# Performance work log

Hardware: AMD Instinct MI355X
Metric: run time of the kernel (lower is better)

## Reference

```python
import jax, jax.numpy as jnp
import numpy as np
from jax import tree_util as jtu

B, N, DIM = 2, 2048, 512
HEADS, DH = 4, 128
CHUNK = 64
NC = N // CHUNK
DHID = 4 * DH  # expansion_factor 4
MAX_LR = 1.0   # default_step_transform_max_lr


def rms_norm(x, g, eps=1e-6):
    var = jnp.mean(jnp.square(x), axis=-1, keepdims=True)
    return x * jax.lax.rsqrt(var + eps) * g


def mem_model(params, x):
    # ResidualNorm(MemoryMLP depth=2): out = mlp(rmsnorm(x)) + x
    g, w1, w2 = params
    h = rms_norm(x, g)
    h = jax.nn.gelu(jnp.dot(h, w1), approximate=False)
    h = jnp.dot(h, w2)
    return h + x


def _expand(a, leaf):
    # broadcast a per-(b*h) scalar gate over a weight leaf
    return a.reshape(a.shape + (1,) * (leaf.ndim - 1))


def neural_memory(seq, g_store, g_retrieve, Wq, Wk, Wv, Wa, ba, Wm, Wd, bd, Wg, Wc, mem_g, w1, w2):
    xs = rms_norm(seq, g_store)      # store_norm
    xr = rms_norm(seq, g_retrieve)   # retrieve_norm

    def split_heads(t):
        return t.reshape(B, N, HEADS, DH).transpose(0, 2, 1, 3)  # b h n d

    k = split_heads(xs @ Wk)
    v = split_heads(xs @ Wv)
    q = split_heads(xr @ Wq)

    # adaptive per-token lr (sigmoid * max_lr)
    lr = (jax.nn.sigmoid(xs @ Wa + ba) * MAX_LR).transpose(0, 2, 1)  # [B,H,N]
    # per-chunk pooled stats drive momentum + decay gates (AveragePool)
    pooled = xs.reshape(B, NC, CHUNK, DIM).mean(axis=2)              # [B,NC,DIM]
    beta = jax.nn.sigmoid(pooled @ Wm)                               # momentum factor [B,NC,H]
    alpha = 1.0 - jax.nn.sigmoid(pooled @ Wd + bd)                   # weight-retain (1-decay)

    BH = B * HEADS
    k_c = k.reshape(BH, NC, CHUNK, DH)
    v_c = v.reshape(BH, NC, CHUNK, DH)
    q_c = q.reshape(BH, NC, CHUNK, DH)
    lr_c = lr.reshape(BH, NC, CHUNK)
    beta_t = beta.transpose(0, 2, 1).reshape(BH, NC).T   # [NC,BH]
    alpha_t = alpha.transpose(0, 2, 1).reshape(BH, NC).T

    # per-head memory params repeated over batch*heads (per_head_learned_parameters)
    init_params = (
        jnp.broadcast_to(mem_g, (B, HEADS, DH)).reshape(BH, DH),
        jnp.broadcast_to(w1, (B, HEADS, DH, DHID)).reshape(BH, DH, DHID),
        jnp.broadcast_to(w2, (B, HEADS, DHID, DH)).reshape(BH, DHID, DH),
    )

    def chunk_loss(params, kc, vc, lrc):
        pred = mem_model(params, kc)                              # [CHUNK,DH]
        return jnp.sum(jnp.mean(jnp.square(pred - vc), axis=-1) * lrc)

    # per-chunk 'surprise' gradients: vmap over (b*h) and chunks, grads wrt init weights
    grad_fn = jax.grad(chunk_loss)
    grads = jax.vmap(jax.vmap(grad_fn, in_axes=(None, 0, 0, 0)), in_axes=(0, 0, 0, 0))(
        init_params, k_c, v_c, lr_c)
    sur_t = jtu.tree_map(lambda g: jnp.moveaxis(-g, 1, 0), grads)  # [NC,BH,...]

    # momentum recurrence: m_t = beta_t * m_{t-1} + surprise_t
    def mom_step(m, inp):
        b, s = inp
        m = jtu.tree_map(lambda mm, ss: _expand(b, mm) * mm + ss, m, s)
        return m, m
    m0 = jtu.tree_map(lambda t: jnp.zeros_like(t[0]), sur_t)
    _, upd_t = jax.lax.scan(mom_step, m0, (beta_t, sur_t))

    # weight recurrence with decay: w_t = (1-decay_t) * w_{t-1} + m_t
    def w_step(w, inp):
        a, u = inp
        w = jtu.tree_map(lambda ww, uu: _expand(a, ww) * ww + uu, w, u)
        return w, w
    _, w_t = jax.lax.scan(w_step, init_params, (alpha_t, upd_t))

    # causal retrieval: chunk i reads weights updated through chunk i-1
    w_prev = jtu.tree_map(
        lambda wt, w0: jnp.moveaxis(jnp.concatenate([w0[None], wt[:-1]], axis=0), 0, 1),
        w_t, init_params)                                          # [BH,NC,...]

    retrieved = jax.vmap(jax.vmap(mem_model))(w_prev, q_c)         # [BH,NC,CHUNK,DH]
    retrieved = retrieved.reshape(B, HEADS, N, DH)
    gate = jax.nn.sigmoid(xr @ Wg).transpose(0, 2, 1)[..., None]   # retrieve_gate [B,H,N,1]
    retrieved = retrieved * gate
    out = retrieved.transpose(0, 2, 1, 3).reshape(B, N, HEADS * DH) @ Wc  # combine_heads
    return out


def setup_inputs():
    key = jax.random.key(0)
    ks = jax.random.split(key, 12)
    s = 0.02
    f = jnp.float32
    return {
        "seq": jax.random.normal(ks[0], (B, N, DIM), f),
        "g_store": jnp.ones((DIM,), f),
        "g_retrieve": jnp.ones((DIM,), f),
        "Wq": jax.random.normal(ks[1], (DIM, HEADS * DH), f) * s,
        "Wk": jax.random.normal(ks[2], (DIM, HEADS * DH), f) * s,
        "Wv": jax.random.normal(ks[3], (DIM, HEADS * DH), f) * s,
        "Wa": jax.random.normal(ks[4], (DIM, HEADS), f) * s,
        "ba": jnp.zeros((HEADS,), f),
        "Wm": jax.random.normal(ks[5], (DIM, HEADS), f) * s,
        "Wd": jax.random.normal(ks[6], (DIM, HEADS), f) * s,
        "bd": jnp.zeros((HEADS,), f),
        "Wg": jax.random.normal(ks[7], (DIM, HEADS), f) * s,
        "Wc": jax.random.normal(ks[8], (HEADS * DH, DIM), f) * s,
        "mem_g": jnp.ones((DH,), f),
        "w1": jax.random.normal(ks[9], (DH, DHID), f) * (1.0 / np.sqrt(DH)),
        "w2": jax.random.normal(ks[10], (DHID, DH), f) * (1.0 / np.sqrt(DHID)),
    }


def reference(seq, g_store, g_retrieve, Wq, Wk, Wv, Wa, ba, Wm, Wd, bd, Wg, Wc, mem_g, w1, w2):
    return neural_memory(seq, g_store, g_retrieve, Wq, Wk, Wv, Wa, ba, Wm, Wd, bd, Wg, Wc, mem_g, w1, w2)
```

## Files before the change

### kernel.cpp

```cpp
#include <hip/hip_runtime.h>
#include <hip/hip_bf16.h>

#define B_ 2
#define N_ 2048
#define DIM_ 512
#define H_ 4
#define DH_ 128
#define DHID_ 512
#define CH_ 64
#define NC_ 32
#define BH_ 8

typedef __bf16 bf16x8 __attribute__((ext_vector_type(8)));
typedef float f32x4 __attribute__((ext_vector_type(4)));

__device__ __forceinline__ f32x4 MFMA(bf16x8 a, bf16x8 b, f32x4 c) {
    return __builtin_amdgcn_mfma_f32_16x16x32_bf16(a, b, c, 0, 0, 0);
}
__device__ __forceinline__ bf16x8 ld8(const __bf16* p) { return *(const bf16x8*)p; }

__device__ __forceinline__ float sigmoidf_(float x) { return 1.0f / (1.0f + expf(-x)); }

__device__ __forceinline__ float gelu_f(float x) {
    float x2 = x * x;
    float u = x * fmaf(0.0713548163f, x2, 1.5957691216f);
    float E = __expf(u);
    float r = __builtin_amdgcn_rcpf(E + 1.0f);
    return x * (1.0f - r);
}
__device__ __forceinline__ void gelu_fg(float x, float& f, float& g) {
    float x2 = x * x;
    float u = x * fmaf(0.0713548163f, x2, 1.5957691216f);
    float E = __expf(u);
    float r = __builtin_amdgcn_rcpf(E + 1.0f);
    float omr = 1.0f - r;
    f = x * omr;
    float th = 1.0f - 2.0f * r;
    float ap = fmaf(0.1070322244f, x2, 0.7978845608f);
    g = fmaf(0.5f * x * (1.0f - th * th), ap, omr);
}

__global__ __launch_bounds__(256) void rms_kernel(
    const float* __restrict__ seq, const float* __restrict__ gs,
    const float* __restrict__ gr, const float* __restrict__ Wa,
    const float* __restrict__ ba, const float* __restrict__ Wg,
    float* __restrict__ xs,
    __bf16* __restrict__ xsb, __bf16* __restrict__ xrb,
    float* __restrict__ lrb, float* __restrict__ gateb)
{
    const int row = blockIdx.x;
    const int t = threadIdx.x;
    const int wave = t >> 6, lane = t & 63;
    const float* x = seq + (size_t)row * DIM_;
    float v0 = x[t], v1 = x[t + 256];
    float ss = v0 * v0 + v1 * v1;
#pragma unroll
    for (int off = 32; off; off >>= 1) ss += __shfl_xor(ss, off);
    __shared__ float red[4];
    __shared__ float red2[4][8];
    if (lane == 0) red[wave] = ss;
    __syncthreads();
    float tot = red[0] + red[1] + red[2] + red[3];
    float r = rsqrtf(tot * (1.0f / DIM_) + 1e-6f);
    size_t o = (size_t)row * DIM_;
    float a0 = v0 * r * gs[t], a1 = v1 * r * gs[t + 256];
    float b0 = v0 * r * gr[t], b1 = v1 * r * gr[t + 256];
    xs[o + t] = a0; xs[o + t + 256] = a1;
    xsb[o + t] = (__bf16)a0; xsb[o + t + 256] = (__bf16)a1;
    xrb[o + t] = (__bf16)b0; xrb[o + t + 256] = (__bf16)b1;
    float pa[4], pg[4];
#pragma unroll
    for (int h = 0; h < 4; ++h) {
        pa[h] = a0 * Wa[t * 4 + h] + a1 * Wa[(t + 256) * 4 + h];
        pg[h] = b0 * Wg[t * 4 + h] + b1 * Wg[(t + 256) * 4 + h];
    }
#pragma unroll
    for (int h = 0; h < 4; ++h)
#pragma unroll
        for (int off = 32; off; off >>= 1) {
            pa[h] += __shfl_xor(pa[h], off);
            pg[h] += __shfl_xor(pg[h], off);
        }
    if (lane == 0) {
#pragma unroll
        for (int h = 0; h < 4; ++h) {
            red2[wave][h] = pa[h];
            red2[wave][4 + h] = pg[h];
        }
    }
    __syncthreads();
    if (t < 8) {
        float s = red2[0][t] + red2[1][t] + red2[2][t] + red2[3][t];
        int b = row >> 11, n = row & 2047;
        if (t < 4) lrb[(size_t)(b * 4 + t) * N_ + n] = sigmoidf_(s + ba[t]);
        else gateb[(size_t)(b * 4 + (t - 4)) * N_ + n] = sigmoidf_(s);
    }
}

__global__ __launch_bounds__(256) void ba_kernel(
    const float* __restrict__ xs, const float* __restrict__ Wm,
    const float* __restrict__ Wd, const float* __restrict__ bd,
    float* __restrict__ beta, float* __restrict__ alpha)
{
    const int b = blockIdx.x >> 5, ci = blockIdx.x & 31;
    const int t = threadIdx.x;
    const int wave = t >> 6, lane = t & 63;
    const float* base = xs + ((size_t)b * N_ + ci * CH_) * DIM_;
    const int d0 = t * 2;
    float s0 = 0.f, s1 = 0.f;
#pragma unroll 8
    for (int r = 0; r < CH_; ++r) {
        s0 += base[(size_t)r * DIM_ + d0];
        s1 += base[(size_t)r * DIM_ + d0 + 1];
    }
    s0 *= (1.0f / CH_); s1 *= (1.0f / CH_);
    float pm[4], pd[4];
#pragma unroll
    for (int h = 0; h < 4; ++h) {
        pm[h] = s0 * Wm[d0 * 4 + h] + s1 * Wm[(d0 + 1) * 4 + h];
        pd[h] = s0 * Wd[d0 * 4 + h] + s1 * Wd[(d0 + 1) * 4 + h];
    }
#pragma unroll
    for (int h = 0; h < 4; ++h)
#pragma unroll
        for (int off = 32; off; off >>= 1) {
            pm[h] += __shfl_xor(pm[h], off);
            pd[h] += __shfl_xor(pd[h], off);
        }
    __shared__ float red2[4][8];
    if (lane == 0) {
#pragma unroll
        for (int h = 0; h < 4; ++h) {
            red2[wave][h] = pm[h];
            red2[wave][4 + h] = pd[h];
        }
    }
    __syncthreads();
    if (t < 4) {
        float sm = red2[0][t] + red2[1][t] + red2[2][t] + red2[3][t];
        float sd = red2[0][4 + t] + red2[1][4 + t] + red2[2][4 + t] + red2[3][4 + t];
        int bh = b * 4 + t;
        beta[bh * NC_ + ci] = sigmoidf_(sm);
        alpha[bh * NC_ + ci] = 1.0f - sigmoidf_(sd + bd[t]);
    }
}

__global__ __launch_bounds__(256) void prep_kernel(
    const float* __restrict__ w1, const float* __restrict__ w2,
    const float* __restrict__ Wq, const float* __restrict__ Wk,
    const float* __restrict__ Wv, const float* __restrict__ Wc,
    __bf16* __restrict__ w1b, __bf16* __restrict__ w1Tb,
    __bf16* __restrict__ w2b, __bf16* __restrict__ w2Tb,
    __bf16* __restrict__ WqT, __bf16* __restrict__ WkT,
    __bf16* __restrict__ WvT, __bf16* __restrict__ WcT)
{
    int idx = blockIdx.x * 256 + threadIdx.x;
    if (idx < 65536) {
        w1b[idx] = (__bf16)w1[idx];
        int j = idx >> 7, d = idx & 127;
        w1Tb[idx] = (__bf16)w1[(size_t)d * DHID_ + j];
        w2b[idx] = (__bf16)w2[idx];
        int d2 = idx >> 9, j2 = idx & 511;
        w2Tb[idx] = (__bf16)w2[(size_t)j2 * DH_ + d2];
    }
    int n = idx >> 9, k = idx & 511;
    WqT[idx] = (__bf16)Wq[(size_t)k * 512 + n];
    WkT[idx] = (__bf16)Wk[(size_t)k * 512 + n];
    WvT[idx] = (__bf16)Wv[(size_t)k * 512 + n];
    WcT[idx] = (__bf16)Wc[(size_t)k * 512 + n];
}

__global__ __launch_bounds__(256, 4) void proj_kernel(
    const __bf16* __restrict__ xsb, const __bf16* __restrict__ xrb,
    const __bf16* __restrict__ WqT, const __bf16* __restrict__ WkT,
    const __bf16* __restrict__ WvT,
    float* __restrict__ qb, float* __restrict__ kb, float* __restrict__ vb)
{
    const int z = blockIdx.z;
    const __bf16* A = (z == 0) ? xrb : xsb;
    const __bf16* WT = (z == 0) ? WqT : (z == 1 ? WkT : WvT);
    float* out = (z == 0) ? qb : (z == 1 ? kb : vb);
    const int t = threadIdx.x;
    const int wave = t >> 6, lane = t & 63;
    const int lrow = lane & 15, lgrp = lane >> 4;
    const int c0 = blockIdx.x * 64 + wave * 16;
    const int col0 = blockIdx.y * 64;
    f32x4 acc[4];
#pragma unroll
    for (int i = 0; i < 4; ++i) acc[i] = (f32x4)0.f;
    const __bf16* ar = A + (size_t)(c0 + lrow) * 512;
#pragma unroll 4
    for (int k0 = 0; k0 < 512; k0 += 32) {
        bf16x8 av = ld8(ar + k0 + lgrp * 8);
#pragma unroll
        for (int ct = 0; ct < 4; ++ct) {
            bf16x8 bv = ld8(WT + (size_t)(col0 + ct * 16 + lrow) * 512 + k0 + lgrp * 8);
            acc[ct] = MFMA(av, bv, acc[ct]);
        }
    }
#pragma unroll
    for (int ct = 0; ct < 4; ++ct)
#pragma unroll
        for (int r = 0; r < 4; ++r) {
            int row = c0 + lgrp * 4 + r, col = col0 + ct * 16 + lrow;
            int b = row >> 11, n = row & 2047, h = col >> 7, d = col & 127;
            out[((((size_t)(b * H_ + h) * NC_ + (n >> 6)) * CH_) + (n & 63)) * DH_ + d] = acc[ct][r];
        }
}

__global__ __launch_bounds__(256, 4) void gemm_out(
    const __bf16* __restrict__ A, const __bf16* __restrict__ WT, float* __restrict__ out)
{
    const int t = threadIdx.x;
    const int wave = t >> 6, lane = t & 63;
    const int lrow = lane & 15, lgrp = lane >> 4;
    const int c0 = blockIdx.x * 64 + wave * 16;
    const int col0 = blockIdx.y * 64;
    f32x4 acc[4];
#pragma unroll
    for (int i = 0; i < 4; ++i) acc[i] = (f32x4)0.f;
    const __bf16* ar = A + (size_t)(c0 + lrow) * 512;
#pragma unroll 4
    for (int k0 = 0; k0 < 512; k0 += 32) {
        bf16x8 av = ld8(ar + k0 + lgrp * 8);
#pragma unroll
        for (int ct = 0; ct < 4; ++ct) {
            bf16x8 bv = ld8(WT + (size_t)(col0 + ct * 16 + lrow) * 512 + k0 + lgrp * 8);
            acc[ct] = MFMA(av, bv, acc[ct]);
        }
    }
#pragma unroll
    for (int ct = 0; ct < 4; ++ct)
#pragma unroll
        for (int r = 0; r < 4; ++r) {
            int row = c0 + lgrp * 4 + r, col = col0 + ct * 16 + lrow;
            out[(size_t)row * 512 + col] = acc[ct][r];
        }
}

__global__ __launch_bounds__(1024) void grad_kernel(
    const float* __restrict__ kbuf, const float* __restrict__ vbuf,
    const float* __restrict__ lrbuf, const float* __restrict__ memg,
    const __bf16* __restrict__ w1b, const __bf16* __restrict__ w1Tb,
    const __bf16* __restrict__ w2b, const __bf16* __restrict__ w2Tb,
    float* __restrict__ sg, __bf16* __restrict__ sw1, __bf16* __restrict__ sw2)
{
    const int blk = blockIdx.x;
    const int t = threadIdx.x;
    const int w = t >> 6, lane = t & 63;
    const int lrow = lane & 15, lgrp = lane >> 4;
    const int bh = blk >> 5, nc = blk & 31;
    const float* kc = kbuf + (size_t)blk * (CH_ * DH_);
    const float* vc = vbuf + (size_t)blk * (CH_ * DH_);
    const float* lrp = lrbuf + (size_t)bh * N_ + nc * CH_;
    __bf16* sw1_blk = sw1 + (size_t)blk * (DHID_ * DH_);
    __bf16* sw2_blk = sw2 + (size_t)blk * (DHID_ * DH_);

    __shared__ __bf16 h_s[64][136];
    __shared__ __bf16 e_s[64][136];
    __shared__ __bf16 a_s[64][136];
    __shared__ __bf16 dz_s[64][136];
    __shared__ __bf16 hT_s[128][72];
    __shared__ __bf16 eT_s[128][72];
    __shared__ __bf16 aT_s[128][72];
    __shared__ __bf16 dzT_s[128][72];
    __shared__ float r_s[64];
    __shared__ float lr_s[64];
    __shared__ float g_s[128];
    __shared__ float part_s[2][128];

    if (t < 128) g_s[t] = memg[t];
    if (t < 64) lr_s[t] = lrp[t];
    {
        const int c = t >> 4, i8 = t & 15, d0 = i8 * 8;
        float xv[8];
        float ss = 0.f;
#pragma unroll
        for (int i = 0; i < 2; ++i) {
            float4 f = *(const float4*)(kc + (size_t)c * DH_ + d0 + i * 4);
            xv[i * 4 + 0] = f.x; xv[i * 4 + 1] = f.y; xv[i * 4 + 2] = f.z; xv[i * 4 + 3] = f.w;
            ss += f.x * f.x + f.y * f.y + f.z * f.z + f.w * f.w;
        }
        ss += __shfl_xor(ss, 1); ss += __shfl_xor(ss, 2);
        ss += __shfl_xor(ss, 4); ss += __shfl_xor(ss, 8);
        float r = rsqrtf(ss * (1.0f / DH_) + 1e-6f);
        if (i8 == 0) r_s[c] = r;
        __syncthreads();
#pragma unroll
        for (int i = 0; i < 8; ++i)
            h_s[c][d0 + i] = (__bf16)(xv[i] * r * g_s[d0 + i]);
    }
    __syncthreads();
    {
        const int d = t >> 3, c0 = (t & 7) * 8;
#pragma unroll
        for (int i = 0; i < 8; ++i) hT_s[d][c0 + i] = h_s[c0 + i][d];
    }
    __syncthreads();

    const int cs = w & 3, dq = w >> 2;
    const int c0w = cs * 16, q0 = dq * 32;
    f32x4 yacc[2];
    yacc[0] = (f32x4)0.f; yacc[1] = (f32x4)0.f;

    bf16x8 w1r[8], w2r[8];
#pragma unroll
    for (int kt = 0; kt < 4; ++kt)
#pragma unroll
        for (int ct = 0; ct < 2; ++ct)
            w1r[kt * 2 + ct] = ld8(w1Tb + (size_t)(q0 + ct * 16 + lrow) * 128 + kt * 32 + lgrp * 8);

    for (int jt = 0; jt < 4; ++jt) {
        f32x4 zacc[2];
        zacc[0] = (f32x4)0.f; zacc[1] = (f32x4)0.f;
#pragma unroll
        for (int kt = 0; kt < 4; ++kt) {
            bf16x8 av = ld8(&h_s[c0w + lrow][kt * 32 + lgrp * 8]);
            zacc[0] = MFMA(av, w1r[kt * 2 + 0], zacc[0]);
            zacc[1] = MFMA(av, w1r[kt * 2 + 1], zacc[1]);
        }
#pragma unroll
        for (int kt = 0; kt < 4; ++kt)
#pragma unroll
            for (int ct = 0; ct < 2; ++ct)
                w2r[kt * 2 + ct] = ld8(w2Tb + (size_t)(q0 + ct * 16 + lrow) * 512 + jt * 128 + kt * 32 + lgrp * 8);
#pragma unroll
        for (int ct = 0; ct < 2; ++ct)
#pragma unroll
            for (int r = 0; r < 4; ++r)
                a_s[c0w + lgrp * 4 + r][q0 + ct * 16 + lrow] = (__bf16)gelu_f(zacc[ct][r]);
        __syncthreads();
#pragma unroll
        for (int kt = 0; kt < 4; ++kt) {
            bf16x8 av = ld8(&a_s[c0w + lrow][kt * 32 + lgrp * 8]);
            yacc[0] = MFMA(av, w2r[kt * 2 + 0], yacc[0]);
            yacc[1] = MFMA(av, w2r[kt * 2 + 1], yacc[1]);
        }
        if (jt < 3) {
#pragma unroll
            for (int kt = 0; kt < 4; ++kt)
#pragma unroll
                for (int ct = 0; ct < 2; ++ct)
                    w1r[kt * 2 + ct] = ld8(w1Tb + (size_t)((jt + 1) * 128 + q0 + ct * 16 + lrow) * 128 + kt * 32 + lgrp * 8);
        }
        __syncthreads();
    }
#pragma unroll
    for (int ct = 0; ct < 2; ++ct)
#pragma unroll
        for (int r = 0; r < 4; ++r) {
            int c = c0w + lgrp * 4 + r, d = q0 + ct * 16 + lrow;
            float xvv = kc[(size_t)c * DH_ + d];
            float vvv = vc[(size_t)c * DH_ + d];
            float e = lr_s[c] * (2.0f / DH_) * (yacc[ct][r] + xvv - vvv);
            e_s[c][d] = (__bf16)e;
            eT_s[d][c] = (__bf16)e;
        }
    __syncthreads();

    const int js = w & 7, chh = w >> 3;
    f32x4 dhacc[2];
    dhacc[0] = (f32x4)0.f; dhacc[1] = (f32x4)0.f;

    bf16x8 azr[4], adr[4], w1br[4];
#pragma unroll
    for (int kt = 0; kt < 4; ++kt) {
        azr[kt] = ld8(w1Tb + (size_t)(js * 16 + lrow) * 128 + kt * 32 + lgrp * 8);
        adr[kt] = ld8(w2b + (size_t)(js * 16 + lrow) * 128 + kt * 32 + lgrp * 8);
    }

    for (int jt = 0; jt < 4; ++jt) {
        f32x4 ztacc[2], dtacc[2];
        ztacc[0] = (f32x4)0.f; ztacc[1] = (f32x4)0.f;
        dtacc[0] = (f32x4)0.f; dtacc[1] = (f32x4)0.f;
#pragma unroll
        for (int kt = 0; kt < 4; ++kt) {
#pragma unroll
            for (int ct = 0; ct < 2; ++ct) {
                bf16x8 bvh = ld8(&h_s[chh * 32 + ct * 16 + lrow][kt * 32 + lgrp * 8]);
                bf16x8 bve = ld8(&e_s[chh * 32 + ct * 16 + lrow][kt * 32 + lgrp * 8]);
                ztacc[ct] = MFMA(azr[kt], bvh, ztacc[ct]);
                dtacc[ct] = MFMA(adr[kt], bve, dtacc[ct]);
            }
        }
#pragma unroll
        for (int kt = 0; kt < 4; ++kt)
            w1br[kt] = ld8(w1b + (size_t)(js * 16 + lrow) * 512 + jt * 128 + kt * 32 + lgrp * 8);
#pragma unroll
        for (int ct = 0; ct < 2; ++ct)
#pragma unroll
            for (int r = 0; r < 4; ++r) {
                int j = js * 16 + lgrp * 4 + r, c = chh * 32 + ct * 16 + lrow;
                float zt = ztacc[ct][r];
                float gf, gg;
                gelu_fg(zt, gf, gg);
                aT_s[j][c] = (__bf16)gf;
                float dzt = dtacc[ct][r] * gg;
                dzT_s[j][c] = (__bf16)dzt;
                dz_s[c][j] = (__bf16)dzt;
            }
        __syncthreads();
        {
            f32x4 wacc[4];
#pragma unroll
            for (int i = 0; i < 4; ++i) wacc[i] = (f32x4)0.f;
#pragma unroll
            for (int kt = 0; kt < 2; ++kt) {
                bf16x8 av = ld8(&dzT_s[js * 16 + lrow][kt * 32 + lgrp * 8]);
#pragma unroll
                for (int ct = 0; ct < 4; ++ct) {
                    bf16x8 bv = ld8(&hT_s[chh * 64 + ct * 16 + lrow][kt * 32 + lgrp * 8]);
                    wacc[ct] = MFMA(av, bv, wacc[ct]);
                }
            }
#pragma unroll
            for (int ct = 0; ct < 4; ++ct)
#pragma unroll
                for (int r = 0; r < 4; ++r) {
                    int jg = jt * 128 + js * 16 + lgrp * 4 + r, d = chh * 64 + ct * 16 + lrow;
                    sw1_blk[(size_t)jg * 128 + d] = (__bf16)(-wacc[ct][r]);
                }
        }
        {
            f32x4 wacc[4];
#pragma unroll
            for (int i = 0; i < 4; ++i) wacc[i] = (f32x4)0.f;
#pragma unroll
            for (int kt = 0; kt < 2; ++kt) {
                bf16x8 av = ld8(&eT_s[js * 16 + lrow][kt * 32 + lgrp * 8]);
#pragma unroll
                for (int ct = 0; ct < 4; ++ct) {
                    bf16x8 bv = ld8(&aT_s[chh * 64 + ct * 16 + lrow][kt * 32 + lgrp * 8]);
                    wacc[ct] = MFMA(av, bv, wacc[ct]);
                }
            }
#pragma unroll
            for (int ct = 0; ct < 4; ++ct)
#pragma unroll
                for (int r = 0; r < 4; ++r) {
                    int d = js * 16 + lgrp * 4 + r, jg = jt * 128 + chh * 64 + ct * 16 + lrow;
                    sw2_blk[(size_t)d * 512 + jg] = (__bf16)(-wacc[ct][r]);
                }
        }
#pragma unroll
        for (int kt = 0; kt < 4; ++kt) {
#pragma unroll
            for (int ct = 0; ct < 2; ++ct) {
                bf16x8 bv = ld8(&dz_s[chh * 32 + ct * 16 + lrow][kt * 32 + lgrp * 8]);
                dhacc[ct] = MFMA(w1br[kt], bv, dhacc[ct]);
            }
        }
        if (jt < 3) {
#pragma unroll
            for (int kt = 0; kt < 4; ++kt) {
                azr[kt] = ld8(w1Tb + (size_t)((jt + 1) * 128 + js * 16 + lrow) * 128 + kt * 32 + lgrp * 8);
                adr[kt] = ld8(w2b + (size_t)((jt + 1) * 128 + js * 16 + lrow) * 128 + kt * 32 + lgrp * 8);
            }
        }
        __syncthreads();
    }
    {
        float s[4] = {0.f, 0.f, 0.f, 0.f};
#pragma unroll
        for (int ct = 0; ct < 2; ++ct)
#pragma unroll
            for (int r = 0; r < 4; ++r) {
                int d = js * 16 + lgrp * 4 + r, c = chh * 32 + ct * 16 + lrow;
                s[r] += dhacc[ct][r] * (float)hT_s[d][c];
            }
#pragma unroll
        for (int r = 0; r < 4; ++r) {
            s[r] += __shfl_xor(s[r], 1); s[r] += __shfl_xor(s[r], 2);
            s[r] += __shfl_xor(s[r], 4); s[r] += __shfl_xor(s[r], 8);
        }
        if (lrow == 0) {
#pragma unroll
            for (int r = 0; r < 4; ++r) part_s[chh][js * 16 + lgrp * 4 + r] = s[r];
        }
        __syncthreads();
        if (t < 128) sg[(size_t)blk * DH_ + t] = -(part_s[0][t] + part_s[1][t]) / g_s[t];
    }
}

__global__ __launch_bounds__(256) void scan_all(
    __bf16* __restrict__ sw1, const __bf16* __restrict__ w1T,
    __bf16* __restrict__ sw2, const __bf16* __restrict__ w2T,
    float* __restrict__ sgb, const float* __restrict__ memg,
    const float* __restrict__ beta, const float* __restrict__ alpha)
{
    const int bi = blockIdx.x, t = threadIdx.x;
    if (bi < 512) {
        __bf16* buf = (bi < 256) ? sw1 : sw2;
        const __bf16* init = (bi < 256) ? w1T : w2T;
        int idx = (bi & 255) * 256 + t;
        int bh = idx >> 13, e8 = idx & 8191;
        size_t off = (size_t)e8 * 8;
        const float* bp = beta + bh * NC_;
        const float* ap = alpha + bh * NC_;
        __bf16* base = buf + (size_t)bh * NC_ * 65536 + off;
        bf16x8 iv = *(const bf16x8*)(init + off);
        float m[8], wv[8];
#pragma unroll
        for (int k = 0; k < 8; ++k) { m[k] = 0.f; wv[k] = (float)iv[k]; }
        for (int ci = 0; ci < NC_; ++ci) {
            bf16x8 s = *(const bf16x8*)(base + (size_t)ci * 65536);
            float bb = bp[ci], aa = ap[ci];
            bf16x8 o;
#pragma unroll
            for (int k = 0; k < 8; ++k) {
                o[k] = (__bf16)wv[k];
                m[k] = fmaf(bb, m[k], (float)s[k]);
                wv[k] = fmaf(aa, wv[k], m[k]);
            }
            *(bf16x8*)(base + (size_t)ci * 65536) = o;
        }
    } else {
        int idx = (bi - 512) * 256 + t;
        int bh = idx >> 7, el = idx & 127;
        float wv = memg[el], m = 0.f;
        const float* bp = beta + bh * NC_;
        const float* ap = alpha + bh * NC_;
        float* base = sgb + ((size_t)bh * NC_) * 128 + el;
        for (int ci = 0; ci < NC_; ++ci) {
            float s = base[(size_t)ci * 128];
            base[(size_t)ci * 128] = wv;
            m = fmaf(bp[ci], m, s);
            wv = fmaf(ap[ci], wv, m);
        }
    }
}

__global__ __launch_bounds__(512, 4) void retrieve_kernel(
    const float* __restrict__ qbuf, const float* __restrict__ gatebuf,
    const float* __restrict__ sg, const __bf16* __restrict__ sw1,
    const __bf16* __restrict__ sw2, __bf16* __restrict__ retgb)
{
    const int blk = blockIdx.x;
    const int t = threadIdx.x;
    const int w = t >> 6, lane = t & 63;
    const int lrow = lane & 15, lgrp = lane >> 4;
    const int bh = blk >> 5, nc = blk & 31;
    const float* qc = qbuf + (size_t)blk * (CH_ * DH_);
    const __bf16* w1p = sw1 + (size_t)blk * (DHID_ * DH_);
    const __bf16* w2p = sw2 + (size_t)blk * (DHID_ * DH_);
    const float* gp = sg + (size_t)blk * DH_;

    __shared__ __bf16 h_s[64][136];
    __shared__ __bf16 a_s[64][136];
    __shared__ float g_s[128];

    if (t < 128) g_s[t] = gp[t];
    {
        const int c = t >> 3, dblk = t & 7, d0 = dblk * 16;
        float xv[16];
        float ss = 0.f;
#pragma unroll
        for (int i = 0; i < 4; ++i) {
            float4 f = *(const float4*)(qc + (size_t)c * DH_ + d0 + i * 4);
            xv[i * 4 + 0] = f.x; xv[i * 4 + 1] = f.y; xv[i * 4 + 2] = f.z; xv[i * 4 + 3] = f.w;
            ss += f.x * f.x + f.y * f.y + f.z * f.z + f.w * f.w;
        }
        ss += __shfl_xor(ss, 1); ss += __shfl_xor(ss, 2); ss += __shfl_xor(ss, 4);
        float r = rsqrtf(ss * (1.0f / DH_) + 1e-6f);
        __syncthreads();
#pragma unroll
        for (int i = 0; i < 16; ++i)
            h_s[c][d0 + i] = (__bf16)(xv[i] * r * g_s[d0 + i]);
    }
    __syncthreads();

    const int cs = w & 3, dh2 = w >> 2;
    const int c0w = cs * 16, d0w = dh2 * 64;
    f32x4 yacc[4];
#pragma unroll
    for (int i = 0; i < 4; ++i) yacc[i] = (f32x4)0.f;

    for (int jt = 0; jt < 4; ++jt) {
        f32x4 zacc[4];
#pragma unroll
        for (int i = 0; i < 4; ++i) zacc[i] = (f32x4)0.f;
#pragma unroll
        for (int kt = 0; kt < 4; ++kt) {
            bf16x8 av = ld8(&h_s[c0w + lrow][kt * 32 + lgrp * 8]);
#pragma unroll
            for (int ct = 0; ct < 4; ++ct) {
                int j = jt * 128 + d0w + ct * 16 + lrow;
                bf16x8 bv = ld8(w1p + (size_t)j * 128 + kt * 32 + lgrp * 8);
                zacc[ct] = MFMA(av, bv, zacc[ct]);
            }
        }
#pragma unroll
        for (int ct = 0; ct < 4; ++ct)
#pragma unroll
            for (int r = 0; r < 4; ++r)
                a_s[c0w + lgrp * 4 + r][d0w + ct * 16 + lrow] = (__bf16)gelu_f(zacc[ct][r]);
        __syncthreads();
#pragma unroll
        for (int kt = 0; kt < 4; ++kt) {
            bf16x8 av = ld8(&a_s[c0w + lrow][kt * 32 + lgrp * 8]);
#pragma unroll
            for (int ct = 0; ct < 4; ++ct) {
                int d = d0w + ct * 16 + lrow;
                bf16x8 bv = ld8(w2p + (size_t)d * 512 + jt * 128 + kt * 32 + lgrp * 8);
                yacc[ct] = MFMA(av, bv, yacc[ct]);
            }
        }
        __syncthreads();
    }
    const int b = bh >> 2, hh = bh & 3;
#pragma unroll
    for (int ct = 0; ct < 4; ++ct)
#pragma unroll
        for (int r = 0; r < 4; ++r) {
            int c = c0w + lgrp * 4 + r, d = d0w + ct * 16 + lrow;
            int n = nc * CH_ + c;
            float q = qc[(size_t)c * DH_ + d];
            float gv = gatebuf[(size_t)bh * N_ + n];
            retgb[((size_t)(b * N_ + n)) * 512 + hh * 128 + d] = (__bf16)((yacc[ct][r] + q) * gv);
        }
}

extern "C" void kernel_launch(void* const* d_in, const int* in_sizes, int n_in,
                              void* d_out, int out_size, void* d_ws, size_t ws_size,
                              hipStream_t stream) {
    const float* seq     = (const float*)d_in[0];
    const float* g_store = (const float*)d_in[1];
    const float* g_retr  = (const float*)d_in[2];
    const float* Wq = (const float*)d_in[3];
    const float* Wk = (const float*)d_in[4];
    const float* Wv = (const float*)d_in[5];
    const float* Wa = (const float*)d_in[6];
    const float* ba = (const float*)d_in[7];
    const float* Wm = (const float*)d_in[8];
    const float* Wd = (const float*)d_in[9];
    const float* bd = (const float*)d_in[10];
    const float* Wg = (const float*)d_in[11];
    const float* Wc = (const float*)d_in[12];
    const float* memg = (const float*)d_in[13];
    const float* w1 = (const float*)d_in[14];
    const float* w2 = (const float*)d_in[15];
    float* out = (float*)d_out;

    float* p = (float*)d_ws;
    float* xs = p;     p += (size_t)B_ * N_ * DIM_;
    float* kb = p;     p += (size_t)B_ * N_ * DIM_;
    float* vb = p;     p += (size_t)B_ * N_ * DIM_;
    float* qb = p;     p += (size_t)B_ * N_ * DIM_;
    float* lrb = p;    p += (size_t)BH_ * N_;
    float* gateb = p;  p += (size_t)BH_ * N_;
    float* beta = p;   p += BH_ * NC_;
    float* alpha = p;  p += BH_ * NC_;
    float* sgb = p;    p += (size_t)BH_ * NC_ * DH_;

    __bf16* bp_ = (__bf16*)p;
    __bf16* xsb = bp_;  bp_ += (size_t)B_ * N_ * DIM_;
    __bf16* xrb = bp_;  bp_ += (size_t)B_ * N_ * DIM_;
    __bf16* retgb = bp_; bp_ += (size_t)B_ * N_ * DIM_;
    __bf16* w1b = bp_;  bp_ += DH_ * DHID_;
    __bf16* w1Tb = bp_; bp_ += DH_ * DHID_;
    __bf16* w2b = bp_;  bp_ += DH_ * DHID_;
    __bf16* w2Tb = bp_; bp_ += DH_ * DHID_;
    __bf16* WqT = bp_;  bp_ += DIM_ * DIM_;
    __bf16* WkT = bp_;  bp_ += DIM_ * DIM_;
    __bf16* WvT = bp_;  bp_ += DIM_ * DIM_;
    __bf16* WcT = bp_;  bp_ += DIM_ * DIM_;
    __bf16* sw1b = bp_; bp_ += (size_t)BH_ * NC_ * DH_ * DHID_;
    __bf16* sw2b = bp_; bp_ += (size_t)BH_ * NC_ * DH_ * DHID_;

    rms_kernel<<<B_ * N_, 256, 0, stream>>>(seq, g_store, g_retr, Wa, ba, Wg,
                                            xs, xsb, xrb, lrb, gateb);
    ba_kernel<<<B_ * NC_, 256, 0, stream>>>(xs, Wm, Wd, bd, beta, alpha);
    prep_kernel<<<1024, 256, 0, stream>>>(w1, w2, Wq, Wk, Wv, Wc,
                                          w1b, w1Tb, w2b, w2Tb, WqT, WkT, WvT, WcT);
    proj_kernel<<<dim3(64, 8, 3), 256, 0, stream>>>(xsb, xrb, WqT, WkT, WvT, qb, kb, vb);
    grad_kernel<<<BH_ * NC_, 1024, 0, stream>>>(kb, vb, lrb, memg, w1b, w1Tb, w2b, w2Tb,
                                                sgb, sw1b, sw2b);
    scan_all<<<516, 256, 0, stream>>>(sw1b, w1Tb, sw2b, w2Tb, sgb, memg, beta, alpha);
    retrieve_kernel<<<BH_ * NC_, 512, 0, stream>>>(qb, gateb, sgb, sw1b, sw2b, retgb);
    gemm_out<<<dim3(64, 8), 256, 0, stream>>>(retgb, WcT, out);
}
```

Measured before the change: 315.3 us.

## Split grad kernel into hprep, forward and backward kernels with doubled block counts

Replaces the monolithic 256-block grad kernel with three kernels: a normalization prep that writes h and its transpose to global bf16 buffers, a forward kernel that computes the error over half-chunks (512 blocks), and a backward kernel that computes weight gradients over half of the hidden dimension (512 blocks). The aim is more parallelism and lower per-block shared memory on a 256-CU-class GPU, where the old kernel ran only one 1024-thread block per chunk. The norm-gain gradient is now computed algebraically from w1 times the w1 gradient, not from dh, with two partial buffers summed inside the scan. The cost is extra global round-trips for h, e and their transposes, plus two more launches.

After: 474.6 us. +50.5%, slower.

```diff
diff --git a/kernel.cpp b/kernel.cpp
--- a/kernel.cpp
+++ b/kernel.cpp
@@ -238,166 +238,168 @@
         }
 }
 
-__global__ __launch_bounds__(1024) void grad_kernel(
-    const float* __restrict__ kbuf, const float* __restrict__ vbuf,
-    const float* __restrict__ lrbuf, const float* __restrict__ memg,
-    const __bf16* __restrict__ w1b, const __bf16* __restrict__ w1Tb,
-    const __bf16* __restrict__ w2b, const __bf16* __restrict__ w2Tb,
-    float* __restrict__ sg, __bf16* __restrict__ sw1, __bf16* __restrict__ sw2)
+__global__ __launch_bounds__(256) void hprep_kernel(
+    const float* __restrict__ kbuf, const float* __restrict__ memg,
+    __bf16* __restrict__ hb, __bf16* __restrict__ hTb)
 {
     const int blk = blockIdx.x;
+    const int t = threadIdx.x;
+    __shared__ __bf16 h_s[64][130];
+    __shared__ float g_s[128];
+    if (t < 128) g_s[t] = memg[t];
+    const int c = t >> 2, q = t & 3, d0 = q * 32;
+    const float* kc = kbuf + (size_t)blk * 8192 + (size_t)c * 128 + d0;
+    float xv[32];
+    float ss = 0.f;
+#pragma unroll
+    for (int i = 0; i < 8; ++i) {
+        float4 f = *(const float4*)(kc + i * 4);
+        xv[i * 4 + 0] = f.x; xv[i * 4 + 1] = f.y; xv[i * 4 + 2] = f.z; xv[i * 4 + 3] = f.w;
+        ss += f.x * f.x + f.y * f.y + f.z * f.z + f.w * f.w;
+    }
+    ss += __shfl_xor(ss, 1); ss += __shfl_xor(ss, 2);
+    float r = rsqrtf(ss * (1.0f / DH_) + 1e-6f);
+    __syncthreads();
+    bf16x8 pk[4];
+#pragma unroll
+    for (int i = 0; i < 32; ++i) {
+        __bf16 hv = (__bf16)(xv[i] * r * g_s[d0 + i]);
+        h_s[c][d0 + i] = hv;
+        pk[i >> 3][i & 7] = hv;
+    }
+    __bf16* hrow = hb + (size_t)blk * 8192 + (size_t)c * 128 + d0;
+#pragma unroll
+    for (int i = 0; i < 4; ++i) *(bf16x8*)(hrow + i * 8) = pk[i];
+    __syncthreads();
+    const int d = t >> 1, c0 = (t & 1) * 32;
+#pragma unroll
+    for (int i = 0; i < 4; ++i) {
+        bf16x8 o;
+#pragma unroll
+        for (int k = 0; k < 8; ++k) o[k] = h_s[c0 + i * 8 + k][d];
+        *(bf16x8*)(hTb + (size_t)blk * 8192 + (size_t)d * 64 + c0 + i * 8) = o;
+    }
+}
+
+__global__ __launch_bounds__(1024, 8) void gradfwd_kernel(
+    const __bf16* __restrict__ hb, const float* __restrict__ kbuf,
+    const float* __restrict__ vbuf, const float* __restrict__ lrbuf,
+    const __bf16* __restrict__ w1Tb, const __bf16* __restrict__ w2Tb,
+    __bf16* __restrict__ eb, __bf16* __restrict__ eTb)
+{
+    const int bi = blockIdx.x;
+    const int blk = bi >> 1, chalf = bi & 1;
     const int t = threadIdx.x;
     const int w = t >> 6, lane = t & 63;
     const int lrow = lane & 15, lgrp = lane >> 4;
     const int bh = blk >> 5, nc = blk & 31;
-    const float* kc = kbuf + (size_t)blk * (CH_ * DH_);
-    const float* vc = vbuf + (size_t)blk * (CH_ * DH_);
-    const float* lrp = lrbuf + (size_t)bh * N_ + nc * CH_;
+
+    __shared__ __bf16 a_s[32][516];
+    __shared__ float lr_s[32];
+    if (t < 32) lr_s[t] = lrbuf[(size_t)bh * N_ + nc * CH_ + chalf * 32 + t];
+
+    const __bf16* hblk = hb + (size_t)blk * 8192 + (size_t)chalf * 32 * 128;
+
+    {
+        const int cs = w & 1, jq = w >> 1;
+        const int j0 = jq * 64;
+        f32x4 zacc[4];
+#pragma unroll
+        for (int i = 0; i < 4; ++i) zacc[i] = (f32x4)0.f;
+#pragma unroll
+        for (int kt = 0; kt < 4; ++kt) {
+            bf16x8 av = ld8(hblk + (size_t)(cs * 16 + lrow) * 128 + kt * 32 + lgrp * 8);
+#pragma unroll
+            for (int ct = 0; ct < 4; ++ct) {
+                bf16x8 bv = ld8(w1Tb + (size_t)(j0 + ct * 16 + lrow) * 128 + kt * 32 + lgrp * 8);
+                zacc[ct] = MFMA(av, bv, zacc[ct]);
+            }
+        }
+#pragma unroll
+        for (int ct = 0; ct < 4; ++ct)
+#pragma unroll
+            for (int r = 0; r < 4; ++r)
+                a_s[cs * 16 + lgrp * 4 + r][j0 + ct * 16 + lrow] = (__bf16)gelu_f(zacc[ct][r]);
+    }
+    __syncthreads();
+
+    {
+        const int cs = w & 1, dq = w >> 1;
+        const int d0 = dq * 16;
+        f32x4 yacc = (f32x4)0.f;
+#pragma unroll
+        for (int kt = 0; kt < 16; ++kt) {
+            bf16x8 av = ld8(&a_s[cs * 16 + lrow][kt * 32 + lgrp * 8]);
+            bf16x8 bv = ld8(w2Tb + (size_t)(d0 + lrow) * 512 + kt * 32 + lgrp * 8);
+            yacc = MFMA(av, bv, yacc);
+        }
+        const int d = d0 + lrow;
+#pragma unroll
+        for (int r = 0; r < 4; ++r) {
+            int cl = cs * 16 + lgrp * 4 + r;
+            int cc = chalf * 32 + cl;
+            float kv = kbuf[(size_t)blk * 8192 + (size_t)cc * 128 + d];
+            float vv = vbuf[(size_t)blk * 8192 + (size_t)cc * 128 + d];
+            float e = lr_s[cl] * (2.0f / DH_) * (yacc[r] + kv - vv);
+            eb[(size_t)blk * 8192 + (size_t)cc * 128 + d] = (__bf16)e;
+            eTb[(size_t)blk * 8192 + (size_t)d * 64 + cc] = (__bf16)e;
+        }
+    }
+}
+
+__global__ __launch_bounds__(1024, 8) void gradbwd_kernel(
+    const __bf16* __restrict__ hb, const __bf16* __restrict__ hTb,
+    const __bf16* __restrict__ eb, const __bf16* __restrict__ eTb,
+    const __bf16* __restrict__ w1b, const __bf16* __restrict__ w1Tb,
+    const __bf16* __restrict__ w2b,
+    __bf16* __restrict__ sw1, __bf16* __restrict__ sw2,
+    float* __restrict__ sgpA, float* __restrict__ sgpB)
+{
+    const int bi = blockIdx.x;
+    const int blk = bi >> 1, jhalf = bi & 1;
+    const int t = threadIdx.x;
+    const int w = t >> 6, lane = t & 63;
+    const int lrow = lane & 15, lgrp = lane >> 4;
+    const int js = w & 7, chh = w >> 3;
+    const __bf16* hblk = hb + (size_t)blk * 8192;
+    const __bf16* eblk = eb + (size_t)blk * 8192;
+    const __bf16* hTblk = hTb + (size_t)blk * 8192;
+    const __bf16* eTblk = eTb + (size_t)blk * 8192;
     __bf16* sw1_blk = sw1 + (size_t)blk * (DHID_ * DH_);
     __bf16* sw2_blk = sw2 + (size_t)blk * (DHID_ * DH_);
 
-    __shared__ __bf16 h_s[64][136];
-    __shared__ __bf16 e_s[64][136];
-    __shared__ __bf16 a_s[64][136];
-    __shared__ __bf16 dz_s[64][136];
-    __shared__ __bf16 hT_s[128][72];
-    __shared__ __bf16 eT_s[128][72];
-    __shared__ __bf16 aT_s[128][72];
-    __shared__ __bf16 dzT_s[128][72];
-    __shared__ float r_s[64];
-    __shared__ float lr_s[64];
-    __shared__ float g_s[128];
-    __shared__ float part_s[2][128];
-
-    if (t < 128) g_s[t] = memg[t];
-    if (t < 64) lr_s[t] = lrp[t];
-    {
-        const int c = t >> 4, i8 = t & 15, d0 = i8 * 8;
-        float xv[8];
-        float ss = 0.f;
-#pragma unroll
-        for (int i = 0; i < 2; ++i) {
-            float4 f = *(const float4*)(kc + (size_t)c * DH_ + d0 + i * 4);
-            xv[i * 4 + 0] = f.x; xv[i * 4 + 1] = f.y; xv[i * 4 + 2] = f.z; xv[i * 4 + 3] = f.w;
-            ss += f.x * f.x + f.y * f.y + f.z * f.z + f.w * f.w;
-        }
-        ss += __shfl_xor(ss, 1); ss += __shfl_xor(ss, 2);
-        ss += __shfl_xor(ss, 4); ss += __shfl_xor(ss, 8);
-        float r = rsqrtf(ss * (1.0f / DH_) + 1e-6f);
-        if (i8 == 0) r_s[c] = r;
-        __syncthreads();
-#pragma unroll
-        for (int i = 0; i < 8; ++i)
-            h_s[c][d0 + i] = (__bf16)(xv[i] * r * g_s[d0 + i]);
-    }
-    __syncthreads();
-    {
-        const int d = t >> 3, c0 = (t & 7) * 8;
-#pragma unroll
-        for (int i = 0; i < 8; ++i) hT_s[d][c0 + i] = h_s[c0 + i][d];
-    }
-    __syncthreads();
-
-    const int cs = w & 3, dq = w >> 2;
-    const int c0w = cs * 16, q0 = dq * 32;
-    f32x4 yacc[2];
-    yacc[0] = (f32x4)0.f; yacc[1] = (f32x4)0.f;
-
-    bf16x8 w1r[8], w2r[8];
-#pragma unroll
-    for (int kt = 0; kt < 4; ++kt)
-#pragma unroll
-        for (int ct = 0; ct < 2; ++ct)
-            w1r[kt * 2 + ct] = ld8(w1Tb + (size_t)(q0 + ct * 16 + lrow) * 128 + kt * 32 + lgrp * 8);
-
-    for (int jt = 0; jt < 4; ++jt) {
-        f32x4 zacc[2];
-        zacc[0] = (f32x4)0.f; zacc[1] = (f32x4)0.f;
-#pragma unroll
-        for (int kt = 0; kt < 4; ++kt) {
-            bf16x8 av = ld8(&h_s[c0w + lrow][kt * 32 + lgrp * 8]);
-            zacc[0] = MFMA(av, w1r[kt * 2 + 0], zacc[0]);
-            zacc[1] = MFMA(av, w1r[kt * 2 + 1], zacc[1]);
-        }
-#pragma unroll
-        for (int kt = 0; kt < 4; ++kt)
-#pragma unroll
-            for (int ct = 0; ct < 2; ++ct)
-                w2r[kt * 2 + ct] = ld8(w2Tb + (size_t)(q0 + ct * 16 + lrow) * 512 + jt * 128 + kt * 32 + lgrp * 8);
-#pragma unroll
-        for (int ct = 0; ct < 2; ++ct)
-#pragma unroll
-            for (int r = 0; r < 4; ++r)
-                a_s[c0w + lgrp * 4 + r][q0 + ct * 16 + lrow] = (__bf16)gelu_f(zacc[ct][r]);
-        __syncthreads();
-#pragma unroll
-        for (int kt = 0; kt < 4; ++kt) {
-            bf16x8 av = ld8(&a_s[c0w + lrow][kt * 32 + lgrp * 8]);
-            yacc[0] = MFMA(av, w2r[kt * 2 + 0], yacc[0]);
-            yacc[1] = MFMA(av, w2r[kt * 2 + 1], yacc[1]);
-        }
-        if (jt < 3) {
-#pragma unroll
-            for (int kt = 0; kt < 4; ++kt)
-#pragma unroll
-                for (int ct = 0; ct < 2; ++ct)
-                    w1r[kt * 2 + ct] = ld8(w1Tb + (size_t)((jt + 1) * 128 + q0 + ct * 16 + lrow) * 128 + kt * 32 + lgrp * 8);
-        }
-        __syncthreads();
-    }
-#pragma unroll
-    for (int ct = 0; ct < 2; ++ct)
-#pragma unroll
-        for (int r = 0; r < 4; ++r) {
-            int c = c0w + lgrp * 4 + r, d = q0 + ct * 16 + lrow;
-            float xvv = kc[(size_t)c * DH_ + d];
-            float vvv = vc[(size_t)c * DH_ + d];
-            float e = lr_s[c] * (2.0f / DH_) * (yacc[ct][r] + xvv - vvv);
-            e_s[c][d] = (__bf16)e;
-            eT_s[d][c] = (__bf16)e;
-        }
-    __syncthreads();
-
-    const int js = w & 7, chh = w >> 3;
-    f32x4 dhacc[2];
-    dhacc[0] = (f32x4)0.f; dhacc[1] = (f32x4)0.f;
-
-    bf16x8 azr[4], adr[4], w1br[4];
-#pragma unroll
-    for (int kt = 0; kt < 4; ++kt) {
-        azr[kt] = ld8(w1Tb + (size_t)(js * 16 + lrow) * 128 + kt * 32 + lgrp * 8);
-        adr[kt] = ld8(w2b + (size_t)(js * 16 + lrow) * 128 + kt * 32 + lgrp * 8);
-    }
-
-    for (int jt = 0; jt < 4; ++jt) {
+    __shared__ __bf16 aT_s[128][66];
+    __shared__ __bf16 dzT_s[128][66];
+    __shared__ float part_dg[16][64];
+
+    float dgacc[4] = {0.f, 0.f, 0.f, 0.f};
+
+    for (int jt = jhalf * 2; jt < jhalf * 2 + 2; ++jt) {
+        const int jg0 = jt * 128;
         f32x4 ztacc[2], dtacc[2];
         ztacc[0] = (f32x4)0.f; ztacc[1] = (f32x4)0.f;
         dtacc[0] = (f32x4)0.f; dtacc[1] = (f32x4)0.f;
 #pragma unroll
         for (int kt = 0; kt < 4; ++kt) {
+            bf16x8 avz = ld8(w1Tb + (size_t)(jg0 + js * 16 + lrow) * 128 + kt * 32 + lgrp * 8);
+            bf16x8 avd = ld8(w2b + (size_t)(jg0 + js * 16 + lrow) * 128 + kt * 32 + lgrp * 8);
 #pragma unroll
             for (int ct = 0; ct < 2; ++ct) {
-                bf16x8 bvh = ld8(&h_s[chh * 32 + ct * 16 + lrow][kt * 32 + lgrp * 8]);
-                bf16x8 bve = ld8(&e_s[chh * 32 + ct * 16 + lrow][kt * 32 + lgrp * 8]);
-                ztacc[ct] = MFMA(azr[kt], bvh, ztacc[ct]);
-                dtacc[ct] = MFMA(adr[kt], bve, dtacc[ct]);
-            }
-        }
-#pragma unroll
-        for (int kt = 0; kt < 4; ++kt)
-            w1br[kt] = ld8(w1b + (size_t)(js * 16 + lrow) * 512 + jt * 128 + kt * 32 + lgrp * 8);
+                bf16x8 bvh = ld8(hblk + (size_t)(chh * 32 + ct * 16 + lrow) * 128 + kt * 32 + lgrp * 8);
+                bf16x8 bve = ld8(eblk + (size_t)(chh * 32 + ct * 16 + lrow) * 128 + kt * 32 + lgrp * 8);
+                ztacc[ct] = MFMA(avz, bvh, ztacc[ct]);
+                dtacc[ct] = MFMA(avd, bve, dtacc[ct]);
+            }
+        }
 #pragma unroll
         for (int ct = 0; ct < 2; ++ct)
 #pragma unroll
             for (int r = 0; r < 4; ++r) {
-                int j = js * 16 + lgrp * 4 + r, c = chh * 32 + ct * 16 + lrow;
-                float zt = ztacc[ct][r];
+                int jl = js * 16 + lgrp * 4 + r, c = chh * 32 + ct * 16 + lrow;
                 float gf, gg;
-                gelu_fg(zt, gf, gg);
-                aT_s[j][c] = (__bf16)gf;
-                float dzt = dtacc[ct][r] * gg;
-                dzT_s[j][c] = (__bf16)dzt;
-                dz_s[c][j] = (__bf16)dzt;
+                gelu_fg(ztacc[ct][r], gf, gg);
+                aT_s[jl][c] = (__bf16)gf;
+                dzT_s[jl][c] = (__bf16)(dtacc[ct][r] * gg);
             }
         __syncthreads();
         {
@@ -409,17 +411,20 @@
                 bf16x8 av = ld8(&dzT_s[js * 16 + lrow][kt * 32 + lgrp * 8]);
 #pragma unroll
                 for (int ct = 0; ct < 4; ++ct) {
-                    bf16x8 bv = ld8(&hT_s[chh * 64 + ct * 16 + lrow][kt * 32 + lgrp * 8]);
+                    bf16x8 bv = ld8(hTblk + (size_t)(chh * 64 + ct * 16 + lrow) * 64 + kt * 32 + lgrp * 8);
                     wacc[ct] = MFMA(av, bv, wacc[ct]);
                 }
             }
 #pragma unroll
-            for (int ct = 0; ct < 4; ++ct)
+            for (int ct = 0; ct < 4; ++ct) {
+                int d = chh * 64 + ct * 16 + lrow;
 #pragma unroll
                 for (int r = 0; r < 4; ++r) {
-                    int jg = jt * 128 + js * 16 + lgrp * 4 + r, d = chh * 64 + ct * 16 + lrow;
+                    int jg = jg0 + js * 16 + lgrp * 4 + r;
                     sw1_blk[(size_t)jg * 128 + d] = (__bf16)(-wacc[ct][r]);
+                    dgacc[ct] -= (float)w1Tb[(size_t)jg * 128 + d] * wacc[ct][r];
                 }
+            }
         }
         {
             f32x4 wacc[4];
@@ -427,7 +432,7 @@
             for (int i = 0; i < 4; ++i) wacc[i] = (f32x4)0.f;
 #pragma unroll
             for (int kt = 0; kt < 2; ++kt) {
-                bf16x8 av = ld8(&eT_s[js * 16 + lrow][kt * 32 + lgrp * 8]);
+                bf16x8 av = ld8(eTblk + (size_t)(js * 16 + lrow) * 64 + kt * 32 + lgrp * 8);
 #pragma unroll
                 for (int ct = 0; ct < 4; ++ct) {
                     bf16x8 bv = ld8(&aT_s[chh * 64 + ct * 16 + lrow][kt * 32 + lgrp * 8]);
@@ -438,54 +443,37 @@
             for (int ct = 0; ct < 4; ++ct)
 #pragma unroll
                 for (int r = 0; r < 4; ++r) {
-                    int d = js * 16 + lgrp * 4 + r, jg = jt * 128 + chh * 64 + ct * 16 + lrow;
+                    int d = js * 16 + lgrp * 4 + r, jg = jg0 + chh * 64 + ct * 16 + lrow;
                     sw2_blk[(size_t)d * 512 + jg] = (__bf16)(-wacc[ct][r]);
                 }
         }
-#pragma unroll
-        for (int kt = 0; kt < 4; ++kt) {
-#pragma unroll
-            for (int ct = 0; ct < 2; ++ct) {
-                bf16x8 bv = ld8(&dz_s[chh * 32 + ct * 16 + lrow][kt * 32 + lgrp * 8]);
-                dhacc[ct] = MFMA(w1br[kt], bv, dhacc[ct]);
-            }
-        }
-        if (jt < 3) {
-#pragma unroll
-            for (int kt = 0; kt < 4; ++kt) {
-                azr[kt] = ld8(w1Tb + (size_t)((jt + 1) * 128 + js * 16 + lrow) * 128 + kt * 32 + lgrp * 8);
-                adr[kt] = ld8(w2b + (size_t)((jt + 1) * 128 + js * 16 + lrow) * 128 + kt * 32 + lgrp * 8);
-            }
-        }
         __syncthreads();
     }
-    {
-        float s[4] = {0.f, 0.f, 0.f, 0.f};
-#pragma unroll
-        for (int ct = 0; ct < 2; ++ct)
-#pragma unroll
-            for (int r = 0; r < 4; ++r) {
-                int d = js * 16 + lgrp * 4 + r, c = chh * 32 + ct * 16 + lrow;
-                s[r] += dhacc[ct][r] * (float)hT_s[d][c];
-            }
-#pragma unroll
-        for (int r = 0; r < 4; ++r) {
-            s[r] += __shfl_xor(s[r], 1); s[r] += __shfl_xor(s[r], 2);
-            s[r] += __shfl_xor(s[r], 4); s[r] += __shfl_xor(s[r], 8);
-        }
-        if (lrow == 0) {
-#pragma unroll
-            for (int r = 0; r < 4; ++r) part_s[chh][js * 16 + lgrp * 4 + r] = s[r];
-        }
-        __syncthreads();
-        if (t < 128) sg[(size_t)blk * DH_ + t] = -(part_s[0][t] + part_s[1][t]) / g_s[t];
+#pragma unroll
+    for (int ct = 0; ct < 4; ++ct) {
+        dgacc[ct] += __shfl_xor(dgacc[ct], 16);
+        dgacc[ct] += __shfl_xor(dgacc[ct], 32);
+    }
+    if (lane < 16) {
+#pragma unroll
+        for (int ct = 0; ct < 4; ++ct) part_dg[w][ct * 16 + lane] = dgacc[ct];
+    }
+    __syncthreads();
+    if (t < 128) {
+        int grp = t >> 6;
+        float s = 0.f;
+#pragma unroll
+        for (int j = 0; j < 8; ++j) s += part_dg[grp * 8 + j][t & 63];
+        float* dst = jhalf ? sgpB : sgpA;
+        dst[(size_t)blk * DH_ + t] = s;
     }
 }
 
 __global__ __launch_bounds__(256) void scan_all(
     __bf16* __restrict__ sw1, const __bf16* __restrict__ w1T,
     __bf16* __restrict__ sw2, const __bf16* __restrict__ w2T,
-    float* __restrict__ sgb, const float* __restrict__ memg,
+    float* __restrict__ sgb, const float* __restrict__ sgpB,
+    const float* __restrict__ memg,
     const float* __restrict__ beta, const float* __restrict__ alpha)
 {
     const int bi = blockIdx.x, t = threadIdx.x;
@@ -517,12 +505,15 @@
     } else {
         int idx = (bi - 512) * 256 + t;
         int bh = idx >> 7, el = idx & 127;
-        float wv = memg[el], m = 0.f;
+        float g = memg[el];
+        float rg = 1.0f / g;
+        float wv = g, m = 0.f;
         const float* bp = beta + bh * NC_;
         const float* ap = alpha + bh * NC_;
         float* base = sgb + ((size_t)bh * NC_) * 128 + el;
+        const float* baseB = sgpB + ((size_t)bh * NC_) * 128 + el;
         for (int ci = 0; ci < NC_; ++ci) {
-            float s = base[(size_t)ci * 128];
+            float s = (base[(size_t)ci * 128] + baseB[(size_t)ci * 128]) * rg;
             base[(size_t)ci * 128] = wv;
             m = fmaf(bp[ci], m, s);
             wv = fmaf(ap[ci], wv, m);
@@ -651,11 +642,16 @@
     float* beta = p;   p += BH_ * NC_;
     float* alpha = p;  p += BH_ * NC_;
     float* sgb = p;    p += (size_t)BH_ * NC_ * DH_;
+    float* sgpB = p;   p += (size_t)BH_ * NC_ * DH_;
 
     __bf16* bp_ = (__bf16*)p;
     __bf16* xsb = bp_;  bp_ += (size_t)B_ * N_ * DIM_;
     __bf16* xrb = bp_;  bp_ += (size_t)B_ * N_ * DIM_;
     __bf16* retgb = bp_; bp_ += (size_t)B_ * N_ * DIM_;
+    __bf16* hbuf = bp_; bp_ += (size_t)BH_ * N_ * DH_;
+    __bf16* hTbuf = bp_; bp_ += (size_t)BH_ * N_ * DH_;
+    __bf16* ebuf = bp_; bp_ += (size_t)BH_ * N_ * DH_;
+    __bf16* eTbuf = bp_; bp_ += (size_t)BH_ * N_ * DH_;
     __bf16* w1b = bp_;  bp_ += DH_ * DHID_;
     __bf16* w1Tb = bp_; bp_ += DH_ * DHID_;
     __bf16* w2b = bp_;  bp_ += DH_ * DHID_;
@@ -673,9 +669,13 @@
     prep_kernel<<<1024, 256, 0, stream>>>(w1, w2, Wq, Wk, Wv, Wc,
                                           w1b, w1Tb, w2b, w2Tb, WqT, WkT, WvT, WcT);
     proj_kernel<<<dim3(64, 8, 3), 256, 0, stream>>>(xsb, xrb, WqT, WkT, WvT, qb, kb, vb);
-    grad_kernel<<<BH_ * NC_, 1024, 0, stream>>>(kb, vb, lrb, memg, w1b, w1Tb, w2b, w2Tb,
-                                                sgb, sw1b, sw2b);
-    scan_all<<<516, 256, 0, stream>>>(sw1b, w1Tb, sw2b, w2Tb, sgb, memg, beta, alpha);
+    hprep_kernel<<<BH_ * NC_, 256, 0, stream>>>(kb, memg, hbuf, hTbuf);
+    gradfwd_kernel<<<BH_ * NC_ * 2, 1024, 0, stream>>>(hbuf, kb, vb, lrb, w1Tb, w2Tb,
+                                                       ebuf, eTbuf);
+    gradbwd_kernel<<<BH_ * NC_ * 2, 1024, 0, stream>>>(hbuf, hTbuf, ebuf, eTbuf,
+                                                       w1b, w1Tb, w2b,
+                                                       sw1b, sw2b, sgb, sgpB);
+    scan_all<<<516, 256, 0, stream>>>(sw1b, w1Tb, sw2b, w2Tb, sgb, sgpB, memg, beta, alpha);
     retrieve_kernel<<<BH_ * NC_, 512, 0, stream>>>(qb, gateb, sgb, sw1b, sw2b, retgb);
     gemm_out<<<dim3(64, 8), 256, 0, stream>>>(retgb, WcT, out);
 }
```

## Derive RMSNorm gain gradient from W1 gradient instead of separate dh MFMA pass

Applied to the files above, without the earlier changes.

Computes the gradient for the memory model's norm gain algebraically: each entry of the already-computed W1 gradient is multiplied by the matching W1 weight and summed over the hidden dimension. The old path computed dh = dz·W1ᵀ with extra MFMAs and then reduced it against h. The change drops the dz_s shared buffer, the per-step global loads of w1 rows and those MFMAs. In exchange it adds a scalar global read of w1T for every W1-gradient element plus a cross-wave reduction through shared memory, and the result picks up different rounding because the bf16-rounded weight and fp32 accumulators are used.

Result: slower. 321.6 us (+2.0%).

```diff
diff --git a/kernel.cpp b/kernel.cpp
--- a/kernel.cpp
+++ b/kernel.cpp
@@ -259,15 +259,13 @@
     __shared__ __bf16 h_s[64][136];
     __shared__ __bf16 e_s[64][136];
     __shared__ __bf16 a_s[64][136];
-    __shared__ __bf16 dz_s[64][136];
     __shared__ __bf16 hT_s[128][72];
     __shared__ __bf16 eT_s[128][72];
     __shared__ __bf16 aT_s[128][72];
     __shared__ __bf16 dzT_s[128][72];
-    __shared__ float r_s[64];
     __shared__ float lr_s[64];
     __shared__ float g_s[128];
-    __shared__ float part_s[2][128];
+    __shared__ float part_dg[16][64];
 
     if (t < 128) g_s[t] = memg[t];
     if (t < 64) lr_s[t] = lrp[t];
@@ -284,7 +282,6 @@
         ss += __shfl_xor(ss, 1); ss += __shfl_xor(ss, 2);
         ss += __shfl_xor(ss, 4); ss += __shfl_xor(ss, 8);
         float r = rsqrtf(ss * (1.0f / DH_) + 1e-6f);
-        if (i8 == 0) r_s[c] = r;
         __syncthreads();
 #pragma unroll
         for (int i = 0; i < 8; ++i)
@@ -359,10 +356,9 @@
     __syncthreads();
 
     const int js = w & 7, chh = w >> 3;
-    f32x4 dhacc[2];
-    dhacc[0] = (f32x4)0.f; dhacc[1] = (f32x4)0.f;
-
-    bf16x8 azr[4], adr[4], w1br[4];
+    float dgacc[4] = {0.f, 0.f, 0.f, 0.f};
+
+    bf16x8 azr[4], adr[4];
 #pragma unroll
     for (int kt = 0; kt < 4; ++kt) {
         azr[kt] = ld8(w1Tb + (size_t)(js * 16 + lrow) * 128 + kt * 32 + lgrp * 8);
@@ -384,20 +380,14 @@
             }
         }
 #pragma unroll
-        for (int kt = 0; kt < 4; ++kt)
-            w1br[kt] = ld8(w1b + (size_t)(js * 16 + lrow) * 512 + jt * 128 + kt * 32 + lgrp * 8);
-#pragma unroll
         for (int ct = 0; ct < 2; ++ct)
 #pragma unroll
             for (int r = 0; r < 4; ++r) {
-                int j = js * 16 + lgrp * 4 + r, c = chh * 32 + ct * 16 + lrow;
-                float zt = ztacc[ct][r];
+                int jl = js * 16 + lgrp * 4 + r, c = chh * 32 + ct * 16 + lrow;
                 float gf, gg;
-                gelu_fg(zt, gf, gg);
-                aT_s[j][c] = (__bf16)gf;
-                float dzt = dtacc[ct][r] * gg;
-                dzT_s[j][c] = (__bf16)dzt;
-                dz_s[c][j] = (__bf16)dzt;
+                gelu_fg(ztacc[ct][r], gf, gg);
+                aT_s[jl][c] = (__bf16)gf;
+                dzT_s[jl][c] = (__bf16)(dtacc[ct][r] * gg);
             }
         __syncthreads();
         {
@@ -414,12 +404,15 @@
                 }
             }
 #pragma unroll
-            for (int ct = 0; ct < 4; ++ct)
+            for (int ct = 0; ct < 4; ++ct) {
+                int d = chh * 64 + ct * 16 + lrow;
 #pragma unroll
                 for (int r = 0; r < 4; ++r) {
-                    int jg = jt * 128 + js * 16 + lgrp * 4 + r, d = chh * 64 + ct * 16 + lrow;
+                    int jg = jt * 128 + js * 16 + lgrp * 4 + r;
                     sw1_blk[(size_t)jg * 128 + d] = (__bf16)(-wacc[ct][r]);
+                    dgacc[ct] -= (float)w1Tb[(size_t)jg * 128 + d] * wacc[ct][r];
                 }
+            }
         }
         {
             f32x4 wacc[4];
@@ -442,14 +435,6 @@
                     sw2_blk[(size_t)d * 512 + jg] = (__bf16)(-wacc[ct][r]);
                 }
         }
-#pragma unroll
-        for (int kt = 0; kt < 4; ++kt) {
-#pragma unroll
-            for (int ct = 0; ct < 2; ++ct) {
-                bf16x8 bv = ld8(&dz_s[chh * 32 + ct * 16 + lrow][kt * 32 + lgrp * 8]);
-                dhacc[ct] = MFMA(w1br[kt], bv, dhacc[ct]);
-            }
-        }
         if (jt < 3) {
 #pragma unroll
             for (int kt = 0; kt < 4; ++kt) {
@@ -459,26 +444,22 @@
         }
         __syncthreads();
     }
-    {
-        float s[4] = {0.f, 0.f, 0.f, 0.f};
-#pragma unroll
-        for (int ct = 0; ct < 2; ++ct)
-#pragma unroll
-            for (int r = 0; r < 4; ++r) {
-                int d = js * 16 + lgrp * 4 + r, c = chh * 32 + ct * 16 + lrow;
-                s[r] += dhacc[ct][r] * (float)hT_s[d][c];
-            }
-#pragma unroll
-        for (int r = 0; r < 4; ++r) {
-            s[r] += __shfl_xor(s[r], 1); s[r] += __shfl_xor(s[r], 2);
-            s[r] += __shfl_xor(s[r], 4); s[r] += __shfl_xor(s[r], 8);
-        }
-        if (lrow == 0) {
-#pragma unroll
-            for (int r = 0; r < 4; ++r) part_s[chh][js * 16 + lgrp * 4 + r] = s[r];
-        }
-        __syncthreads();
-        if (t < 128) sg[(size_t)blk * DH_ + t] = -(part_s[0][t] + part_s[1][t]) / g_s[t];
+#pragma unroll
+    for (int ct = 0; ct < 4; ++ct) {
+        dgacc[ct] += __shfl_xor(dgacc[ct], 16);
+        dgacc[ct] += __shfl_xor(dgacc[ct], 32);
+    }
+    if (lane < 16) {
+#pragma unroll
+        for (int ct = 0; ct < 4; ++ct) part_dg[w][ct * 16 + lane] = dgacc[ct];
+    }
+    __syncthreads();
+    if (t < 128) {
+        int grp = t >> 6;
+        float s = 0.f;
+#pragma unroll
+        for (int j = 0; j < 8; ++j) s += part_dg[grp * 8 + j][t & 63];
+        sg[(size_t)blk * DH_ + t] = s / g_s[t];
     }
 }
 
```
